# Optimization experiments

Hardware: AMD Instinct MI355X
Metric: run time of the kernel (lower is better)

## Reference

```python
import jax, jax.numpy as jnp
import numpy as np

N_NODES = 50000
N_EDGES = 1200000
NODE_DIM = 64
HIDDEN = 64
OUT_DIM = 1
N_LAYERS = 3


def setup_inputs() -> dict:
    key = jax.random.key(0)
    ks = jax.random.split(key, 16)
    inp = {
        "H": jax.random.normal(ks[0], (N_NODES, NODE_DIM), dtype=jnp.float32),
        "edge_index": jax.random.randint(ks[1], (2, N_EDGES), 0, N_NODES, dtype=jnp.int64),
        "E": jax.random.normal(ks[2], (N_EDGES, 16), dtype=jnp.float32),
    }
    # per-layer params: node_encoder (enc) and update_w (upd); weights stored [in, out]
    for i in range(N_LAYERS):
        in_dim = NODE_DIM if i == 0 else HIDDEN
        s = 1.0 / np.sqrt(in_dim)
        inp[f"enc_w{i}"] = jax.random.uniform(ks[3 + 2 * i], (in_dim, HIDDEN), jnp.float32, -s, s)
        inp[f"enc_b{i}"] = jax.random.uniform(ks[4 + 2 * i], (HIDDEN,), jnp.float32, -s, s)
        sh = 1.0 / np.sqrt(HIDDEN)
        inp[f"upd_w{i}"] = jax.random.uniform(ks[9 + 2 * i], (HIDDEN, HIDDEN), jnp.float32, -sh, sh)
        inp[f"upd_b{i}"] = jax.random.uniform(ks[10 + 2 * i], (HIDDEN,), jnp.float32, -sh, sh)
    so = 1.0 / np.sqrt(HIDDEN)
    inp["out_w"] = jax.random.uniform(ks[15], (HIDDEN, OUT_DIM), jnp.float32, -so, so)
    inp["out_b"] = jnp.zeros((OUT_DIM,), jnp.float32)
    return inp


def _gcn_forward(H, edge_index, params):
    u, v = edge_index[0], edge_index[1]
    # symmetric normalization with implicit self-loop degree bump (calc_norm_factor)
    deg = jax.ops.segment_sum(jnp.ones(u.shape[0], H.dtype), u, num_segments=N_NODES) + 1.0
    dis = deg ** -0.5  # deg >= 1, never inf
    norm = dis[u] * dis[v]  # [n_edges]
    for i in range(N_LAYERS):
        enc_w, enc_b, upd_w, upd_b = params[i]
        H = H @ enc_w + enc_b                      # node_encoder
        msgs = norm[:, None] * H[u]                # gather + scale
        agg = jax.ops.segment_sum(msgs, v, num_segments=N_NODES)  # scatter-add
        H = jax.nn.relu((agg + H) @ upd_w + upd_b)  # update + ReLU (dropout = identity in eval)
    return H


def reference(H, edge_index, E, enc_w0, enc_b0, upd_w0, upd_b0, enc_w1, enc_b1,
              upd_w1, upd_b1, enc_w2, enc_b2, upd_w2, upd_b2, out_w, out_b):
    params = [(enc_w0, enc_b0, upd_w0, upd_b0),
              (enc_w1, enc_b1, upd_w1, upd_b1),
              (enc_w2, enc_b2, upd_w2, upd_b2)]
    Hf = _gcn_forward(H, edge_index, params)
    graph_emb = jnp.mean(Hf, axis=0, keepdims=True)  # [1, HIDDEN] readout (batch=None)
    return graph_emb @ out_w + out_b                 # [1, OUT_DIM]
```

## Files before the change

kernel.cpp:

```cpp
#include <hip/hip_runtime.h>
#include <hip/hip_fp16.h>

#define NN 50000
#define NE 1200000
#define DIM 64
#define NB 782
#define BB 196
#define SLICES 512
#define ES 2344
#define VCAP 2048
#define GB 782
#define FRONT_LDS 33792


__device__ __forceinline__ void lsort_body(char* smem, const int* __restrict__ ei,
                                           ushort* __restrict__ usort,
                                           int* __restrict__ ebuf,
                                           int* __restrict__ lpart_u,
                                           int* __restrict__ lpart_v,
                                           int s) {
    int* hist = (int*)smem;
    int* wsum = (int*)(smem + 3136);
    ushort* sbu = (ushort*)(smem + 4160);
    int* sbv = (int*)(smem + 8848);
    int t = threadIdx.x;
    int w = t >> 6, l = t & 63;
    int e0 = s * ES, e1 = min(e0 + ES, NE), len = e1 - e0;
    int i0 = t * 4;

    for (int i = t; i < NB; i += 256) hist[i] = 0;
    __syncthreads();
    for (int e = e0 + t; e < e1; e += 256) atomicAdd(&hist[ei[e] >> 6], 1);
    __syncthreads();
    {
        int h0 = (i0 + 0 < NB) ? hist[i0 + 0] : 0;
        int h1 = (i0 + 1 < NB) ? hist[i0 + 1] : 0;
        int h2 = (i0 + 2 < NB) ? hist[i0 + 2] : 0;
        int h3 = (i0 + 3 < NB) ? hist[i0 + 3] : 0;
        int p1 = h0, p2 = h0 + h1, p3 = p2 + h2, p4 = p3 + h3;
        int inc = p4;
        for (int o = 1; o < 64; o <<= 1) {
            int x = __shfl_up(inc, o, 64);
            if (l >= o) inc += x;
        }
        if (l == 63) wsum[w] = inc;
        __syncthreads();
        int base = 0;
#pragma unroll
        for (int j = 0; j < 4; ++j) if (j < w) base += wsum[j];
        int total = wsum[0] + wsum[1] + wsum[2] + wsum[3];
        int excl = base + inc - p4;
        int* lpu = lpart_u + s * (NB + 1);
        if (i0 + 0 < NB) { lpu[i0 + 0] = excl;      hist[i0 + 0] = excl; }
        if (i0 + 1 < NB) { lpu[i0 + 1] = excl + p1; hist[i0 + 1] = excl + p1; }
        if (i0 + 2 < NB) { lpu[i0 + 2] = excl + p2; hist[i0 + 2] = excl + p2; }
        if (i0 + 3 < NB) { lpu[i0 + 3] = excl + p3; hist[i0 + 3] = excl + p3; }
        if (t == 255) lpu[NB] = total;
    }
    __syncthreads();
    for (int e = e0 + t; e < e1; e += 256) {
        int u = ei[e];
        int pos = atomicAdd(&hist[u >> 6], 1);
        sbu[pos] = (ushort)u;
    }
    __syncthreads();
    for (int i = t; i < len; i += 256) usort[e0 + i] = sbu[i];
    for (int i = t; i < NB; i += 256) hist[i] = 0;
    __syncthreads();

    for (int e = e0 + t; e < e1; e += 256) atomicAdd(&hist[ei[NE + e] >> 6], 1);
    __syncthreads();
    {
        int h0 = (i0 + 0 < NB) ? hist[i0 + 0] : 0;
        int h1 = (i0 + 1 < NB) ? hist[i0 + 1] : 0;
        int h2 = (i0 + 2 < NB) ? hist[i0 + 2] : 0;
        int h3 = (i0 + 3 < NB) ? hist[i0 + 3] : 0;
        int p1 = h0, p2 = h0 + h1, p3 = p2 + h2, p4 = p3 + h3;
        int inc = p4;
        for (int o = 1; o < 64; o <<= 1) {
            int x = __shfl_up(inc, o, 64);
            if (l >= o) inc += x;
        }
        if (l == 63) wsum[w] = inc;
        __syncthreads();
        int base = 0;
#pragma unroll
        for (int j = 0; j < 4; ++j) if (j < w) base += wsum[j];
        int total = wsum[0] + wsum[1] + wsum[2] + wsum[3];
        int excl = base + inc - p4;
        int* lpv = lpart_v + s * (NB + 1);
        if (i0 + 0 < NB) { lpv[i0 + 0] = excl;      hist[i0 + 0] = excl; }
        if (i0 + 1 < NB) { lpv[i0 + 1] = excl + p1; hist[i0 + 1] = excl + p1; }
        if (i0 + 2 < NB) { lpv[i0 + 2] = excl + p2; hist[i0 + 2] = excl + p2; }
        if (i0 + 3 < NB) { lpv[i0 + 3] = excl + p3; hist[i0 + 3] = excl + p3; }
        if (t == 255) lpv[NB] = total;
    }
    __syncthreads();
    for (int e = e0 + t; e < e1; e += 256) {
        int u = ei[e], v = ei[NE + e];
        int pos = atomicAdd(&hist[v >> 6], 1);
        sbv[pos] = u | ((v & 63) << 16);
    }
    __syncthreads();
    for (int i = t; i < len; i += 256) ebuf[e0 + i] = sbv[i];
}

__device__ __forceinline__ void gemm_h_body(char* smem, int blk,
                                            const float* __restrict__ A,
                                            const float* __restrict__ W,
                                            const float* __restrict__ bias,
                                            __half* __restrict__ Ch, int M) {
    float (*As)[68] = (float(*)[68])smem;
    float (*Bs)[64] = (float(*)[64])(smem + 17408);
    int t = threadIdx.x;
    int row0 = blk * 64;
#pragma unroll
    for (int i = 0; i < 4; ++i) {
        int idx = t + i * 256;
        int r = idx >> 4, c = (idx & 15) << 2;
        float4 val = make_float4(0.f, 0.f, 0.f, 0.f);
        if (row0 + r < M) val = *(const float4*)&A[(size_t)(row0 + r) * DIM + c];
        *(float4*)&As[r][c] = val;
        *(float4*)&Bs[r][c] = *(const float4*)&W[r * DIM + c];
    }
    __syncthreads();
    int r0 = (t >> 4) * 4;
    int c0 = (t & 15) * 4;
    float acc[4][4] = {};
#pragma unroll
    for (int k = 0; k < 64; k += 4) {
        float4 b0 = *(float4*)&Bs[k + 0][c0];
        float4 b1 = *(float4*)&Bs[k + 1][c0];
        float4 b2 = *(float4*)&Bs[k + 2][c0];
        float4 b3 = *(float4*)&Bs[k + 3][c0];
#pragma unroll
        for (int i = 0; i < 4; ++i) {
            float4 av = *(float4*)&As[r0 + i][k];
            acc[i][0] = fmaf(av.x, b0.x, fmaf(av.y, b1.x, fmaf(av.z, b2.x, fmaf(av.w, b3.x, acc[i][0]))));
            acc[i][1] = fmaf(av.x, b0.y, fmaf(av.y, b1.y, fmaf(av.z, b2.y, fmaf(av.w, b3.y, acc[i][1]))));
            acc[i][2] = fmaf(av.x, b0.z, fmaf(av.y, b1.z, fmaf(av.z, b2.z, fmaf(av.w, b3.z, acc[i][2]))));
            acc[i][3] = fmaf(av.x, b0.w, fmaf(av.y, b1.w, fmaf(av.z, b2.w, fmaf(av.w, b3.w, acc[i][3]))));
        }
    }
    float4 bv = *(const float4*)&bias[c0];
#pragma unroll
    for (int i = 0; i < 4; ++i) {
        int r = row0 + r0 + i;
        if (r < M) {
            __half2 p0 = __floats2half2_rn(acc[i][0] + bv.x, acc[i][1] + bv.y);
            __half2 p1 = __floats2half2_rn(acc[i][2] + bv.z, acc[i][3] + bv.w);
            uint2 pk;
            pk.x = *(unsigned int*)&p0;
            pk.y = *(unsigned int*)&p1;
            *(uint2*)&Ch[(size_t)r * DIM + c0] = pk;
        }
    }
}

__global__ __launch_bounds__(256) void k_front(const int* __restrict__ ei,
                                               ushort* __restrict__ usort,
                                               int* __restrict__ ebuf,
                                               int* __restrict__ lpart_u,
                                               int* __restrict__ lpart_v,
                                               const float* __restrict__ A,
                                               const float* __restrict__ W,
                                               const float* __restrict__ bias,
                                               __half* __restrict__ Ch) {
    extern __shared__ char smem[];
    int b = blockIdx.x;
    if (b < 256)
        lsort_body(smem, ei, usort, ebuf, lpart_u, lpart_v, b);
    else if (b < 512)
        gemm_h_body(smem, b - 256, A, W, bias, Ch, NN);
    else if (b < 768)
        lsort_body(smem, ei, usort, ebuf, lpart_u, lpart_v, b - 256);
    else
        gemm_h_body(smem, b - 512, A, W, bias, Ch, NN);
}

__global__ __launch_bounds__(256) void k_mid(const ushort* __restrict__ usort,
                                             const int* __restrict__ lpart_u,
                                             float* __restrict__ dis,
                                             float* __restrict__ colsum) {
    __shared__ int sh[4][64];
    int bid = blockIdx.x;
    if (bid == 0 && threadIdx.x < 64) colsum[threadIdx.x] = 0.f;
    int w = threadIdx.x >> 6, l = threadIdx.x & 63;
    int b = bid * 4 + w;
    if (b >= NB) return;
    sh[w][l] = 0;
    __builtin_amdgcn_wave_barrier();
    for (int s = l; s < SLICES; s += 64) {
        const int* row = lpart_u + s * (NB + 1);
        int st = row[b], en = row[b + 1];
        for (int i = st; i < en; ++i)
            atomicAdd(&sh[w][usort[s * ES + i] & 63], 1);
    }
    __builtin_amdgcn_wave_barrier();
    int n = (b << 6) + l;
    if (n < NN) dis[n] = rsqrtf((float)sh[w][l] + 1.0f);
}

__global__ __launch_bounds__(256) void k_vsort(const int* __restrict__ ebuf,
                                               const int* __restrict__ lpart_v,
                                               const float* __restrict__ dis,
                                               int* __restrict__ edges,
                                               int* __restrict__ row_ptr) {
    __shared__ int cache[4][VCAP];
    __shared__ int cnt[4][64];
    __shared__ int cur[4][64];
    int w = threadIdx.x >> 6, l = threadIdx.x & 63;
    int b = blockIdx.x * 4 + w;
    if (b >= NB) return;
    int len[8], st8[8];
    int tl = 0, ts = 0;
#pragma unroll
    for (int k = 0; k < 8; ++k) {
        const int* row = lpart_v + (l * 8 + k) * (NB + 1);
        int st = row[b], en = row[b + 1];
        st8[k] = st;
        len[k] = en - st;
        tl += len[k];
        ts += st;
    }
    int n = tl, rb = ts;
    for (int off = 32; off; off >>= 1) {
        n += __shfl_down(n, off, 64);
        rb += __shfl_down(rb, off, 64);
    }
    n = __shfl(n, 0, 64);
    int rbase = __shfl(rb, 0, 64);
    cnt[w][l] = 0;
    __builtin_amdgcn_wave_barrier();
    if (n <= VCAP) {
        int inc = tl;
        for (int o = 1; o < 64; o <<= 1) {
            int x = __shfl_up(inc, o, 64);
            if (l >= o) inc += x;
        }
        int pos = inc - tl;
#pragma unroll
        for (int k = 0; k < 8; ++k) {
            int s = l * 8 + k;
            int st = st8[k];
            for (int i = 0; i < len[k]; ++i)
                cache[w][pos++] = ebuf[s * ES + st + i];
        }
        __builtin_amdgcn_wave_barrier();
        for (int i = l; i < n; i += 64)
            atomicAdd(&cnt[w][(cache[w][i] >> 16) & 63], 1);
        __builtin_amdgcn_wave_barrier();
        int c = cnt[w][l];
        int inc2 = c;
        for (int o = 1; o < 64; o <<= 1) {
            int x = __shfl_up(inc2, o, 64);
            if (l >= o) inc2 += x;
        }
        int excl = inc2 - c;
        cur[w][l] = rbase + excl;
        row_ptr[(b << 6) + l] = rbase + excl;
        __builtin_amdgcn_wave_barrier();
        for (int i = l; i < n; i += 64) {
            int rec = cache[w][i];
            int u = rec & 0xFFFF;
            int p2 = atomicAdd(&cur[w][(rec >> 16) & 63], 1);
            ushort dh = __half_as_ushort(__float2half_rn(dis[u]));
            edges[p2] = u | ((int)dh << 16);
        }
    } else {
        for (int s = l; s < SLICES; s += 64) {
            const int* row = lpart_v + s * (NB + 1);
            int st = row[b], en = row[b + 1];
            for (int i = st; i < en; ++i)
                atomicAdd(&cnt[w][(ebuf[s * ES + i] >> 16) & 63], 1);
        }
        __builtin_amdgcn_wave_barrier();
        int c = cnt[w][l];
        int inc2 = c;
        for (int o = 1; o < 64; o <<= 1) {
            int x = __shfl_up(inc2, o, 64);
            if (l >= o) inc2 += x;
        }
        int excl = inc2 - c;
        cur[w][l] = rbase + excl;
        row_ptr[(b << 6) + l] = rbase + excl;
        __builtin_amdgcn_wave_barrier();
        for (int s = l; s < SLICES; s += 64) {
            const int* row = lpart_v + s * (NB + 1);
            int st = row[b], en = row[b + 1];
            for (int i = st; i < en; ++i) {
                int rec = ebuf[s * ES + i];
                int u = rec & 0xFFFF;
                int p2 = atomicAdd(&cur[w][(rec >> 16) & 63], 1);
                ushort dh = __half_as_ushort(__float2half_rn(dis[u]));
                edges[p2] = u | ((int)dh << 16);
            }
        }
    }
}

__global__ __launch_bounds__(256) void k_gemm2(const float* __restrict__ X,
                                               const float* __restrict__ W1,
                                               const float* __restrict__ b1,
                                               const float* __restrict__ W2,
                                               const float* __restrict__ b2,
                                               __half* __restrict__ Zh, int M) {
    __shared__ float As[64][68];
    __shared__ float Bs[64][64];
    int t = threadIdx.x;
    int row0 = blockIdx.x * 64;
#pragma unroll
    for (int i = 0; i < 4; ++i) {
        int idx = t + i * 256;
        int r = idx >> 4, c = (idx & 15) << 2;
        float4 val = make_float4(0.f, 0.f, 0.f, 0.f);
        if (row0 + r < M) val = *(const float4*)&X[(size_t)(row0 + r) * DIM + c];
        *(float4*)&As[r][c] = val;
        *(float4*)&Bs[r][c] = *(const float4*)&W1[r * DIM + c];
    }
    __syncthreads();
    int r0 = (t >> 4) * 4;
    int c0 = (t & 15) * 4;
    float acc[4][4] = {};
#pragma unroll
    for (int k = 0; k < 64; k += 4) {
        float4 v0 = *(float4*)&Bs[k + 0][c0];
        float4 v1 = *(float4*)&Bs[k + 1][c0];
        float4 v2 = *(float4*)&Bs[k + 2][c0];
        float4 v3 = *(float4*)&Bs[k + 3][c0];
#pragma unroll
        for (int i = 0; i < 4; ++i) {
            float4 av = *(float4*)&As[r0 + i][k];
            acc[i][0] = fmaf(av.x, v0.x, fmaf(av.y, v1.x, fmaf(av.z, v2.x, fmaf(av.w, v3.x, acc[i][0]))));
            acc[i][1] = fmaf(av.x, v0.y, fmaf(av.y, v1.y, fmaf(av.z, v2.y, fmaf(av.w, v3.y, acc[i][1]))));
            acc[i][2] = fmaf(av.x, v0.z, fmaf(av.y, v1.z, fmaf(av.z, v2.z, fmaf(av.w, v3.z, acc[i][2]))));
            acc[i][3] = fmaf(av.x, v0.w, fmaf(av.y, v1.w, fmaf(av.z, v2.w, fmaf(av.w, v3.w, acc[i][3]))));
        }
    }
    float4 bv1 = *(const float4*)&b1[c0];
    __syncthreads();
#pragma unroll
    for (int i = 0; i < 4; ++i) {
        float4 y;
        y.x = fmaxf(acc[i][0] + bv1.x, 0.f);
        y.y = fmaxf(acc[i][1] + bv1.y, 0.f);
        y.z = fmaxf(acc[i][2] + bv1.z, 0.f);
        y.w = fmaxf(acc[i][3] + bv1.w, 0.f);
        *(float4*)&As[r0 + i][c0] = y;
    }
#pragma unroll
    for (int i = 0; i < 4; ++i) {
        int idx = t + i * 256;
        int r = idx >> 4, c = (idx & 15) << 2;
        *(float4*)&Bs[r][c] = *(const float4*)&W2[r * DIM + c];
    }
    __syncthreads();
    float acc2[4][4] = {};
#pragma unroll
    for (int k = 0; k < 64; k += 4) {
        float4 v0 = *(float4*)&Bs[k + 0][c0];
        float4 v1 = *(float4*)&Bs[k + 1][c0];
        float4 v2 = *(float4*)&Bs[k + 2][c0];
        float4 v3 = *(float4*)&Bs[k + 3][c0];
#pragma unroll
        for (int i = 0; i < 4; ++i) {
            float4 av = *(float4*)&As[r0 + i][k];
            acc2[i][0] = fmaf(av.x, v0.x, fmaf(av.y, v1.x, fmaf(av.z, v2.x, fmaf(av.w, v3.x, acc2[i][0]))));
            acc2[i][1] = fmaf(av.x, v0.y, fmaf(av.y, v1.y, fmaf(av.z, v2.y, fmaf(av.w, v3.y, acc2[i][1]))));
            acc2[i][2] = fmaf(av.x, v0.z, fmaf(av.y, v1.z, fmaf(av.z, v2.z, fmaf(av.w, v3.z, acc2[i][2]))));
            acc2[i][3] = fmaf(av.x, v0.w, fmaf(av.y, v1.w, fmaf(av.z, v2.w, fmaf(av.w, v3.w, acc2[i][3]))));
        }
    }
    float4 bv2 = *(const float4*)&b2[c0];
#pragma unroll
    for (int i = 0; i < 4; ++i) {
        int r = row0 + r0 + i;
        if (r < M) {
            __half2 p0 = __floats2half2_rn(acc2[i][0] + bv2.x, acc2[i][1] + bv2.y);
            __half2 p1 = __floats2half2_rn(acc2[i][2] + bv2.z, acc2[i][3] + bv2.w);
            uint2 pk;
            pk.x = *(unsigned int*)&p0;
            pk.y = *(unsigned int*)&p1;
            *(uint2*)&Zh[(size_t)r * DIM + c0] = pk;
        }
    }
}

__global__ __launch_bounds__(256) void k_gemm_last(const float* __restrict__ A,
                                                   const float* __restrict__ W,
                                                   const float* __restrict__ bias,
                                                   int M, float* __restrict__ colsum) {
    __shared__ float As[64][68];
    __shared__ float Bs[64][64];
    int t = threadIdx.x;
    int row0 = blockIdx.x * 64;
#pragma unroll
    for (int i = 0; i < 4; ++i) {
        int idx = t + i * 256;
        int r = idx >> 4, c = (idx & 15) << 2;
        float4 val = make_float4(0.f, 0.f, 0.f, 0.f);
        if (row0 + r < M) val = *(const float4*)&A[(size_t)(row0 + r) * DIM + c];
        *(float4*)&As[r][c] = val;
        *(float4*)&Bs[r][c] = *(const float4*)&W[r * DIM + c];
    }
    __syncthreads();
    int r0 = (t >> 4) * 4;
    int c0 = (t & 15) * 4;
    float acc[4][4] = {};
#pragma unroll
    for (int k = 0; k < 64; k += 4) {
        float4 b0 = *(float4*)&Bs[k + 0][c0];
        float4 b1 = *(float4*)&Bs[k + 1][c0];
        float4 b2 = *(float4*)&Bs[k + 2][c0];
        float4 b3 = *(float4*)&Bs[k + 3][c0];
#pragma unroll
        for (int i = 0; i < 4; ++i) {
            float4 av = *(float4*)&As[r0 + i][k];
            acc[i][0] = fmaf(av.x, b0.x, fmaf(av.y, b1.x, fmaf(av.z, b2.x, fmaf(av.w, b3.x, acc[i][0]))));
            acc[i][1] = fmaf(av.x, b0.y, fmaf(av.y, b1.y, fmaf(av.z, b2.y, fmaf(av.w, b3.y, acc[i][1]))));
            acc[i][2] = fmaf(av.x, b0.z, fmaf(av.y, b1.z, fmaf(av.z, b2.z, fmaf(av.w, b3.z, acc[i][2]))));
            acc[i][3] = fmaf(av.x, b0.w, fmaf(av.y, b1.w, fmaf(av.z, b2.w, fmaf(av.w, b3.w, acc[i][3]))));
        }
    }
    float4 bv = *(const float4*)&bias[c0];
    float csum[4] = {0.f, 0.f, 0.f, 0.f};
#pragma unroll
    for (int i = 0; i < 4; ++i) {
        int r = row0 + r0 + i;
        if (r < M) {
            csum[0] += fmaxf(acc[i][0] + bv.x, 0.f);
            csum[1] += fmaxf(acc[i][1] + bv.y, 0.f);
            csum[2] += fmaxf(acc[i][2] + bv.z, 0.f);
            csum[3] += fmaxf(acc[i][3] + bv.w, 0.f);
        }
    }
    float* red = &As[0][0];
    __syncthreads();
    *(float4*)&red[(t >> 4) * 64 + c0] = make_float4(csum[0], csum[1], csum[2], csum[3]);
    __syncthreads();
    if (t < 64) {
        float s = 0.f;
#pragma unroll
        for (int g = 0; g < 16; ++g) s += red[g * 64 + t];
        atomicAdd(&colsum[t], s);
    }
}

__global__ __launch_bounds__(256) void k_agg(const uint4* __restrict__ Hq4,
                                             const float* __restrict__ dis,
                                             const int* __restrict__ row_ptr,
                                             const int* __restrict__ edges,
                                             float* __restrict__ X) {
    __shared__ int se[4][64];
    int w = threadIdx.x >> 6, l = threadIdx.x & 63;
    int node = (blockIdx.x << 2) + w;
    if (node >= NN) return;
    int start = row_ptr[node];
    int num = row_ptr[node + 1] - start;
    int g = l >> 3;
    int p = l & 7;
    float4 a0 = {0.f, 0.f, 0.f, 0.f};
    float4 a1 = {0.f, 0.f, 0.f, 0.f};
    for (int base = 0; base < num; base += 64) {
        int lim = min(64, num - base);
        se[w][l] = (l < lim) ? edges[start + base + l] : 0;
        __builtin_amdgcn_wave_barrier();
        int octs = (lim + 7) >> 3;
        int rr[8]; uint4 hh[8];
#pragma unroll
        for (int q = 0; q < 8; ++q)
            if (q < octs) rr[q] = se[w][8 * q + g];
#pragma unroll
        for (int q = 0; q < 8; ++q)
            if (q < octs) hh[q] = Hq4[((rr[q] & 0xFFFF) << 3) + p];
#pragma unroll
        for (int q = 0; q < 8; ++q)
            if (q < octs) {
                float wt = __half2float(__ushort_as_half((ushort)((unsigned)rr[q] >> 16)));
                float2 f0 = __half22float2(*(const __half2*)&hh[q].x);
                float2 f1 = __half22float2(*(const __half2*)&hh[q].y);
                float2 f2 = __half22float2(*(const __half2*)&hh[q].z);
                float2 f3 = __half22float2(*(const __half2*)&hh[q].w);
                a0.x = fmaf(wt, f0.x, a0.x);
                a0.y = fmaf(wt, f0.y, a0.y);
                a0.z = fmaf(wt, f1.x, a0.z);
                a0.w = fmaf(wt, f1.y, a0.w);
                a1.x = fmaf(wt, f2.x, a1.x);
                a1.y = fmaf(wt, f2.y, a1.y);
                a1.z = fmaf(wt, f3.x, a1.z);
                a1.w = fmaf(wt, f3.y, a1.w);
            }
        __builtin_amdgcn_wave_barrier();
    }
#pragma unroll
    for (int m = 8; m < 64; m <<= 1) {
        a0.x += __shfl_xor(a0.x, m, 64);
        a0.y += __shfl_xor(a0.y, m, 64);
        a0.z += __shfl_xor(a0.z, m, 64);
        a0.w += __shfl_xor(a0.w, m, 64);
        a1.x += __shfl_xor(a1.x, m, 64);
        a1.y += __shfl_xor(a1.y, m, 64);
        a1.z += __shfl_xor(a1.z, m, 64);
        a1.w += __shfl_xor(a1.w, m, 64);
    }
    if (g == 0) {
        uint4 sv = Hq4[(node << 3) + p];
        float2 s0 = __half22float2(*(const __half2*)&sv.x);
        float2 s1 = __half22float2(*(const __half2*)&sv.y);
        float2 s2 = __half22float2(*(const __half2*)&sv.z);
        float2 s3 = __half22float2(*(const __half2*)&sv.w);
        float dv = dis[node];
        float4 o0, o1;
        o0.x = fmaf(dv, a0.x, s0.x);
        o0.y = fmaf(dv, a0.y, s0.y);
        o0.z = fmaf(dv, a0.z, s1.x);
        o0.w = fmaf(dv, a0.w, s1.y);
        o1.x = fmaf(dv, a1.x, s2.x);
        o1.y = fmaf(dv, a1.y, s2.y);
        o1.z = fmaf(dv, a1.z, s3.x);
        o1.w = fmaf(dv, a1.w, s3.y);
        float* xr = &X[((size_t)node << 6) + (p << 3)];
        *(float4*)xr = o0;
        *(float4*)(xr + 4) = o1;
    }
}

__global__ void k_out(const float* __restrict__ colsum, const float* __restrict__ out_w,
                      const float* __restrict__ out_b, float* __restrict__ out) {
    int f = threadIdx.x;
    float v = colsum[f] * (1.0f / (float)NN) * out_w[f];
    for (int off = 32; off; off >>= 1) v += __shfl_down(v, off, 64);
    if (f == 0) out[0] = v + out_b[0];
}

extern "C" void kernel_launch(void* const* d_in, const int* in_sizes, int n_in,
                              void* d_out, int out_size, void* d_ws, size_t ws_size,
                              hipStream_t stream) {
    const float* H  = (const float*)d_in[0];
    const int*   ei = (const int*)d_in[1];
    const float* enc_w[3] = { (const float*)d_in[3], (const float*)d_in[7],  (const float*)d_in[11] };
    const float* enc_b[3] = { (const float*)d_in[4], (const float*)d_in[8],  (const float*)d_in[12] };
    const float* upd_w[3] = { (const float*)d_in[5], (const float*)d_in[9],  (const float*)d_in[13] };
    const float* upd_b[3] = { (const float*)d_in[6], (const float*)d_in[10], (const float*)d_in[14] };
    const float* out_w = (const float*)d_in[15];
    const float* out_b = (const float*)d_in[16];
    float* out = (float*)d_out;

    size_t off = 0;
    auto carve = [&](size_t bytes) {
        void* p = (char*)d_ws + off;
        off = (off + bytes + 255) & ~(size_t)255;
        return p;
    };
    int*    lpart_u = (int*)carve((size_t)SLICES * (NB + 1) * 4);
    int*    lpart_v = (int*)carve((size_t)SLICES * (NB + 1) * 4);
    float*  dis     = (float*)carve((size_t)NN * 4);
    ushort* usort   = (ushort*)carve((size_t)SLICES * ES * 2);
    int*    ebuf    = (int*)carve((size_t)SLICES * ES * 4);
    int*    edges   = (int*)carve((size_t)NE * 4);
    int*    row_ptr = (int*)carve((size_t)(NN + 65) * 4);
    __half* Ch      = (__half*)carve((size_t)NN * DIM * 2);
    float*  X       = (float*)carve((size_t)NN * DIM * 4);
    float*  colsum  = (float*)carve(64 * 4);

    const int AB = (NN + 3) / 4;
    const uint4* Hq4 = (const uint4*)Ch;

    k_front<<<512 + GB, 256, FRONT_LDS, stream>>>(ei, usort, ebuf, lpart_u, lpart_v,
                                                  H, enc_w[0], enc_b[0], Ch);
    k_mid<<<BB, 256, 0, stream>>>(usort, lpart_u, dis, colsum);
    k_vsort<<<BB, 256, 0, stream>>>(ebuf, lpart_v, dis, edges, row_ptr);

    k_agg<<<AB, 256, 0, stream>>>(Hq4, dis, row_ptr, edges, X);
    k_gemm2<<<GB, 256, 0, stream>>>(X, upd_w[0], upd_b[0], enc_w[1], enc_b[1], Ch, NN);
    k_agg<<<AB, 256, 0, stream>>>(Hq4, dis, row_ptr, edges, X);
    k_gemm2<<<GB, 256, 0, stream>>>(X, upd_w[1], upd_b[1], enc_w[2], enc_b[2], Ch, NN);
    k_agg<<<AB, 256, 0, stream>>>(Hq4, dis, row_ptr, edges, X);
    k_gemm_last<<<GB, 256, 0, stream>>>(X, upd_w[2], upd_b[2], NN, colsum);

    k_out<<<1, 64, 0, stream>>>(colsum, out_w, out_b, out);
}
```

Baseline: 383.5 us.

## Fuse aggregation into following GEMM and widen mid/vsort to block-per-bucket

Merges the per-node sparse aggregation into the subsequent GEMM kernels, so each 64-row block aggregates its nodes straight into shared memory and the fp32 X buffer no longer goes through global memory. Because a block now reads other nodes' features while writing new ones, the half-precision feature buffer is double-buffered (ChA/ChB). k_mid and k_vsort are also restructured from one bucket per wave to one bucket per 256-thread block, which puts more parallelism on the sorting stage. The cost is that each fused block handles 64 nodes serially per wave (16 each), with fewer blocks and a larger LDS footprint, which may lower latency hiding in the gather.

```diff
diff --git a/kernel.cpp b/kernel.cpp
--- a/kernel.cpp
+++ b/kernel.cpp
@@ -5,7 +5,6 @@
 #define NE 1200000
 #define DIM 64
 #define NB 782
-#define BB 196
 #define SLICES 512
 #define ES 2344
 #define VCAP 2048
@@ -182,23 +181,21 @@
                                              const int* __restrict__ lpart_u,
                                              float* __restrict__ dis,
                                              float* __restrict__ colsum) {
-    __shared__ int sh[4][64];
-    int bid = blockIdx.x;
-    if (bid == 0 && threadIdx.x < 64) colsum[threadIdx.x] = 0.f;
-    int w = threadIdx.x >> 6, l = threadIdx.x & 63;
-    int b = bid * 4 + w;
-    if (b >= NB) return;
-    sh[w][l] = 0;
-    __builtin_amdgcn_wave_barrier();
-    for (int s = l; s < SLICES; s += 64) {
+    __shared__ int sh[64];
+    int b = blockIdx.x;
+    int t = threadIdx.x;
+    if (b == 0 && t < 64) colsum[t] = 0.f;
+    if (t < 64) sh[t] = 0;
+    __syncthreads();
+    for (int s = t; s < SLICES; s += 256) {
         const int* row = lpart_u + s * (NB + 1);
         int st = row[b], en = row[b + 1];
         for (int i = st; i < en; ++i)
-            atomicAdd(&sh[w][usort[s * ES + i] & 63], 1);
-    }
-    __builtin_amdgcn_wave_barrier();
-    int n = (b << 6) + l;
-    if (n < NN) dis[n] = rsqrtf((float)sh[w][l] + 1.0f);
+            atomicAdd(&sh[usort[s * ES + i] & 63], 1);
+    }
+    __syncthreads();
+    int n = (b << 6) + t;
+    if (t < 64 && n < NN) dis[n] = rsqrtf((float)sh[t] + 1.0f);
 }
 
 __global__ __launch_bounds__(256) void k_vsort(const int* __restrict__ ebuf,
@@ -206,92 +203,92 @@
                                                const float* __restrict__ dis,
                                                int* __restrict__ edges,
                                                int* __restrict__ row_ptr) {
-    __shared__ int cache[4][VCAP];
-    __shared__ int cnt[4][64];
-    __shared__ int cur[4][64];
-    int w = threadIdx.x >> 6, l = threadIdx.x & 63;
-    int b = blockIdx.x * 4 + w;
-    if (b >= NB) return;
-    int len[8], st8[8];
-    int tl = 0, ts = 0;
-#pragma unroll
-    for (int k = 0; k < 8; ++k) {
-        const int* row = lpart_v + (l * 8 + k) * (NB + 1);
-        int st = row[b], en = row[b + 1];
-        st8[k] = st;
-        len[k] = en - st;
-        tl += len[k];
-        ts += st;
-    }
-    int n = tl, rb = ts;
-    for (int off = 32; off; off >>= 1) {
-        n += __shfl_down(n, off, 64);
-        rb += __shfl_down(rb, off, 64);
-    }
-    n = __shfl(n, 0, 64);
-    int rbase = __shfl(rb, 0, 64);
-    cnt[w][l] = 0;
-    __builtin_amdgcn_wave_barrier();
+    __shared__ int cache[VCAP];
+    __shared__ int cnt[64];
+    __shared__ int cur[64];
+    __shared__ int wsum[4];
+    __shared__ int rsum[4];
+    int t = threadIdx.x, w = t >> 6, l = t & 63;
+    int b = blockIdx.x;
+    int s0 = t * 2, s1 = t * 2 + 1;
+    const int* r0p = lpart_v + s0 * (NB + 1);
+    const int* r1p = lpart_v + s1 * (NB + 1);
+    int a0 = r0p[b], a1 = r0p[b + 1];
+    int c0 = r1p[b], c1 = r1p[b + 1];
+    int len0 = a1 - a0, len1 = c1 - c0;
+    int tl = len0 + len1;
+    int ts = a0 + c0;
+    int inc = tl;
+    for (int o = 1; o < 64; o <<= 1) {
+        int x = __shfl_up(inc, o, 64);
+        if (l >= o) inc += x;
+    }
+    int tss = ts;
+    for (int off = 32; off; off >>= 1) tss += __shfl_down(tss, off, 64);
+    if (l == 63) wsum[w] = inc;
+    if (l == 0) rsum[w] = tss;
+    if (t < 64) cnt[t] = 0;
+    __syncthreads();
+    int base = 0;
+#pragma unroll
+    for (int j = 0; j < 4; ++j) if (j < w) base += wsum[j];
+    int n = wsum[0] + wsum[1] + wsum[2] + wsum[3];
+    int rbase = rsum[0] + rsum[1] + rsum[2] + rsum[3];
+    int pos = base + inc - tl;
     if (n <= VCAP) {
-        int inc = tl;
-        for (int o = 1; o < 64; o <<= 1) {
-            int x = __shfl_up(inc, o, 64);
-            if (l >= o) inc += x;
-        }
-        int pos = inc - tl;
-#pragma unroll
-        for (int k = 0; k < 8; ++k) {
-            int s = l * 8 + k;
-            int st = st8[k];
-            for (int i = 0; i < len[k]; ++i)
-                cache[w][pos++] = ebuf[s * ES + st + i];
-        }
-        __builtin_amdgcn_wave_barrier();
-        for (int i = l; i < n; i += 64)
-            atomicAdd(&cnt[w][(cache[w][i] >> 16) & 63], 1);
-        __builtin_amdgcn_wave_barrier();
-        int c = cnt[w][l];
-        int inc2 = c;
-        for (int o = 1; o < 64; o <<= 1) {
-            int x = __shfl_up(inc2, o, 64);
-            if (l >= o) inc2 += x;
-        }
-        int excl = inc2 - c;
-        cur[w][l] = rbase + excl;
-        row_ptr[(b << 6) + l] = rbase + excl;
-        __builtin_amdgcn_wave_barrier();
-        for (int i = l; i < n; i += 64) {
-            int rec = cache[w][i];
+        for (int i = 0; i < len0; ++i) cache[pos + i] = ebuf[s0 * ES + a0 + i];
+        int pos1 = pos + len0;
+        for (int i = 0; i < len1; ++i) cache[pos1 + i] = ebuf[s1 * ES + c0 + i];
+        __syncthreads();
+        for (int i = t; i < n; i += 256)
+            atomicAdd(&cnt[(cache[i] >> 16) & 63], 1);
+        __syncthreads();
+        if (w == 0) {
+            int c = cnt[l];
+            int inc2 = c;
+            for (int o = 1; o < 64; o <<= 1) {
+                int x = __shfl_up(inc2, o, 64);
+                if (l >= o) inc2 += x;
+            }
+            int excl = inc2 - c;
+            cur[l] = rbase + excl;
+            row_ptr[(b << 6) + l] = rbase + excl;
+        }
+        __syncthreads();
+        for (int i = t; i < n; i += 256) {
+            int rec = cache[i];
             int u = rec & 0xFFFF;
-            int p2 = atomicAdd(&cur[w][(rec >> 16) & 63], 1);
+            int p2 = atomicAdd(&cur[(rec >> 16) & 63], 1);
             ushort dh = __half_as_ushort(__float2half_rn(dis[u]));
             edges[p2] = u | ((int)dh << 16);
         }
     } else {
-        for (int s = l; s < SLICES; s += 64) {
+        for (int s = t; s < SLICES; s += 256) {
             const int* row = lpart_v + s * (NB + 1);
             int st = row[b], en = row[b + 1];
             for (int i = st; i < en; ++i)
-                atomicAdd(&cnt[w][(ebuf[s * ES + i] >> 16) & 63], 1);
-        }
-        __builtin_amdgcn_wave_barrier();
-        int c = cnt[w][l];
-        int inc2 = c;
-        for (int o = 1; o < 64; o <<= 1) {
-            int x = __shfl_up(inc2, o, 64);
-            if (l >= o) inc2 += x;
-        }
-        int excl = inc2 - c;
-        cur[w][l] = rbase + excl;
-        row_ptr[(b << 6) + l] = rbase + excl;
-        __builtin_amdgcn_wave_barrier();
-        for (int s = l; s < SLICES; s += 64) {
+                atomicAdd(&cnt[(ebuf[s * ES + i] >> 16) & 63], 1);
+        }
+        __syncthreads();
+        if (w == 0) {
+            int c = cnt[l];
+            int inc2 = c;
+            for (int o = 1; o < 64; o <<= 1) {
+                int x = __shfl_up(inc2, o, 64);
+                if (l >= o) inc2 += x;
+            }
+            int excl = inc2 - c;
+            cur[l] = rbase + excl;
+            row_ptr[(b << 6) + l] = rbase + excl;
+        }
+        __syncthreads();
+        for (int s = t; s < SLICES; s += 256) {
             const int* row = lpart_v + s * (NB + 1);
             int st = row[b], en = row[b + 1];
             for (int i = st; i < en; ++i) {
                 int rec = ebuf[s * ES + i];
                 int u = rec & 0xFFFF;
-                int p2 = atomicAdd(&cur[w][(rec >> 16) & 63], 1);
+                int p2 = atomicAdd(&cur[(rec >> 16) & 63], 1);
                 ushort dh = __half_as_ushort(__float2half_rn(dis[u]));
                 edges[p2] = u | ((int)dh << 16);
             }
@@ -299,23 +296,113 @@
     }
 }
 
-__global__ __launch_bounds__(256) void k_gemm2(const float* __restrict__ X,
-                                               const float* __restrict__ W1,
-                                               const float* __restrict__ b1,
-                                               const float* __restrict__ W2,
-                                               const float* __restrict__ b2,
-                                               __half* __restrict__ Zh, int M) {
+__device__ __forceinline__ void agg_body(float (*As)[68], int (*se)[64],
+                                         const uint4* __restrict__ Hq4,
+                                         const float* __restrict__ dis,
+                                         const int* __restrict__ row_ptr,
+                                         const int* __restrict__ edges,
+                                         int row0) {
+    int t = threadIdx.x;
+    int w = t >> 6, l = t & 63;
+    int g = l >> 3;
+    int p = l & 7;
+#pragma unroll 1
+    for (int nn = 0; nn < 16; ++nn) {
+        int node = row0 + (w << 4) + nn;
+        int start = 0, num = 0;
+        if (node < NN) { start = row_ptr[node]; num = row_ptr[node + 1] - start; }
+        float4 a0 = {0.f, 0.f, 0.f, 0.f};
+        float4 a1 = {0.f, 0.f, 0.f, 0.f};
+        for (int base = 0; base < num; base += 64) {
+            int lim = min(64, num - base);
+            se[w][l] = (l < lim) ? edges[start + base + l] : 0;
+            __builtin_amdgcn_wave_barrier();
+            int octs = (lim + 7) >> 3;
+            int rr[8]; uint4 hh[8];
+#pragma unroll
+            for (int q = 0; q < 8; ++q)
+                if (q < octs) rr[q] = se[w][8 * q + g];
+#pragma unroll
+            for (int q = 0; q < 8; ++q)
+                if (q < octs) hh[q] = Hq4[((rr[q] & 0xFFFF) << 3) + p];
+#pragma unroll
+            for (int q = 0; q < 8; ++q)
+                if (q < octs) {
+                    float wt = __half2float(__ushort_as_half((ushort)((unsigned)rr[q] >> 16)));
+                    float2 f0 = __half22float2(*(const __half2*)&hh[q].x);
+                    float2 f1 = __half22float2(*(const __half2*)&hh[q].y);
+                    float2 f2 = __half22float2(*(const __half2*)&hh[q].z);
+                    float2 f3 = __half22float2(*(const __half2*)&hh[q].w);
+                    a0.x = fmaf(wt, f0.x, a0.x);
+                    a0.y = fmaf(wt, f0.y, a0.y);
+                    a0.z = fmaf(wt, f1.x, a0.z);
+                    a0.w = fmaf(wt, f1.y, a0.w);
+                    a1.x = fmaf(wt, f2.x, a1.x);
+                    a1.y = fmaf(wt, f2.y, a1.y);
+                    a1.z = fmaf(wt, f3.x, a1.z);
+                    a1.w = fmaf(wt, f3.y, a1.w);
+                }
+            __builtin_amdgcn_wave_barrier();
+        }
+#pragma unroll
+        for (int m = 8; m < 64; m <<= 1) {
+            a0.x += __shfl_xor(a0.x, m, 64);
+            a0.y += __shfl_xor(a0.y, m, 64);
+            a0.z += __shfl_xor(a0.z, m, 64);
+            a0.w += __shfl_xor(a0.w, m, 64);
+            a1.x += __shfl_xor(a1.x, m, 64);
+            a1.y += __shfl_xor(a1.y, m, 64);
+            a1.z += __shfl_xor(a1.z, m, 64);
+            a1.w += __shfl_xor(a1.w, m, 64);
+        }
+        if (g == 0) {
+            int r = (w << 4) + nn;
+            if (node < NN) {
+                uint4 sv = Hq4[(node << 3) + p];
+                float2 s0 = __half22float2(*(const __half2*)&sv.x);
+                float2 s1 = __half22float2(*(const __half2*)&sv.y);
+                float2 s2 = __half22float2(*(const __half2*)&sv.z);
+                float2 s3 = __half22float2(*(const __half2*)&sv.w);
+                float dv = dis[node];
+                float4 o0, o1;
+                o0.x = fmaf(dv, a0.x, s0.x);
+                o0.y = fmaf(dv, a0.y, s0.y);
+                o0.z = fmaf(dv, a0.z, s1.x);
+                o0.w = fmaf(dv, a0.w, s1.y);
+                o1.x = fmaf(dv, a1.x, s2.x);
+                o1.y = fmaf(dv, a1.y, s2.y);
+                o1.z = fmaf(dv, a1.z, s3.x);
+                o1.w = fmaf(dv, a1.w, s3.y);
+                *(float4*)&As[r][p << 3] = o0;
+                *(float4*)&As[r][(p << 3) + 4] = o1;
+            } else {
+                float4 z = {0.f, 0.f, 0.f, 0.f};
+                *(float4*)&As[r][p << 3] = z;
+                *(float4*)&As[r][(p << 3) + 4] = z;
+            }
+        }
+    }
+}
+
+__global__ __launch_bounds__(256) void k_aggemm2(const uint4* __restrict__ Hq4,
+                                                 const float* __restrict__ dis,
+                                                 const int* __restrict__ row_ptr,
+                                                 const int* __restrict__ edges,
+                                                 const float* __restrict__ W1,
+                                                 const float* __restrict__ b1,
+                                                 const float* __restrict__ W2,
+                                                 const float* __restrict__ b2,
+                                                 __half* __restrict__ Zh) {
     __shared__ float As[64][68];
     __shared__ float Bs[64][64];
+    __shared__ int se[4][64];
     int t = threadIdx.x;
     int row0 = blockIdx.x * 64;
+    agg_body(As, se, Hq4, dis, row_ptr, edges, row0);
 #pragma unroll
     for (int i = 0; i < 4; ++i) {
         int idx = t + i * 256;
         int r = idx >> 4, c = (idx & 15) << 2;
-        float4 val = make_float4(0.f, 0.f, 0.f, 0.f);
-        if (row0 + r < M) val = *(const float4*)&X[(size_t)(row0 + r) * DIM + c];
-        *(float4*)&As[r][c] = val;
         *(float4*)&Bs[r][c] = *(const float4*)&W1[r * DIM + c];
     }
     __syncthreads();
@@ -375,7 +462,7 @@
 #pragma unroll
     for (int i = 0; i < 4; ++i) {
         int r = row0 + r0 + i;
-        if (r < M) {
+        if (r < NN) {
             __half2 p0 = __floats2half2_rn(acc2[i][0] + bv2.x, acc2[i][1] + bv2.y);
             __half2 p1 = __floats2half2_rn(acc2[i][2] + bv2.z, acc2[i][3] + bv2.w);
             uint2 pk;
@@ -386,21 +473,23 @@
     }
 }
 
-__global__ __launch_bounds__(256) void k_gemm_last(const float* __restrict__ A,
-                                                   const float* __restrict__ W,
-                                                   const float* __restrict__ bias,
-                                                   int M, float* __restrict__ colsum) {
+__global__ __launch_bounds__(256) void k_aggemm_last(const uint4* __restrict__ Hq4,
+                                                     const float* __restrict__ dis,
+                                                     const int* __restrict__ row_ptr,
+                                                     const int* __restrict__ edges,
+                                                     const float* __restrict__ W,
+                                                     const float* __restrict__ bias,
+                                                     float* __restrict__ colsum) {
     __shared__ float As[64][68];
     __shared__ float Bs[64][64];
+    __shared__ int se[4][64];
     int t = threadIdx.x;
     int row0 = blockIdx.x * 64;
+    agg_body(As, se, Hq4, dis, row_ptr, edges, row0);
 #pragma unroll
     for (int i = 0; i < 4; ++i) {
         int idx = t + i * 256;
         int r = idx >> 4, c = (idx & 15) << 2;
-        float4 val = make_float4(0.f, 0.f, 0.f, 0.f);
-        if (row0 + r < M) val = *(const float4*)&A[(size_t)(row0 + r) * DIM + c];
-        *(float4*)&As[r][c] = val;
         *(float4*)&Bs[r][c] = *(const float4*)&W[r * DIM + c];
     }
     __syncthreads();
@@ -427,7 +516,7 @@
 #pragma unroll
     for (int i = 0; i < 4; ++i) {
         int r = row0 + r0 + i;
-        if (r < M) {
+        if (r < NN) {
             csum[0] += fmaxf(acc[i][0] + bv.x, 0.f);
             csum[1] += fmaxf(acc[i][1] + bv.y, 0.f);
             csum[2] += fmaxf(acc[i][2] + bv.z, 0.f);
@@ -443,85 +532,6 @@
 #pragma unroll
         for (int g = 0; g < 16; ++g) s += red[g * 64 + t];
         atomicAdd(&colsum[t], s);
-    }
-}
-
-__global__ __launch_bounds__(256) void k_agg(const uint4* __restrict__ Hq4,
-                                             const float* __restrict__ dis,
-                                             const int* __restrict__ row_ptr,
-                                             const int* __restrict__ edges,
-                                             float* __restrict__ X) {
-    __shared__ int se[4][64];
-    int w = threadIdx.x >> 6, l = threadIdx.x & 63;
-    int node = (blockIdx.x << 2) + w;
-    if (node >= NN) return;
-    int start = row_ptr[node];
-    int num = row_ptr[node + 1] - start;
-    int g = l >> 3;
-    int p = l & 7;
-    float4 a0 = {0.f, 0.f, 0.f, 0.f};
-    float4 a1 = {0.f, 0.f, 0.f, 0.f};
-    for (int base = 0; base < num; base += 64) {
-        int lim = min(64, num - base);
-        se[w][l] = (l < lim) ? edges[start + base + l] : 0;
-        __builtin_amdgcn_wave_barrier();
-        int octs = (lim + 7) >> 3;
-        int rr[8]; uint4 hh[8];
-#pragma unroll
-        for (int q = 0; q < 8; ++q)
-            if (q < octs) rr[q] = se[w][8 * q + g];
-#pragma unroll
-        for (int q = 0; q < 8; ++q)
-            if (q < octs) hh[q] = Hq4[((rr[q] & 0xFFFF) << 3) + p];
-#pragma unroll
-        for (int q = 0; q < 8; ++q)
-            if (q < octs) {
-                float wt = __half2float(__ushort_as_half((ushort)((unsigned)rr[q] >> 16)));
-                float2 f0 = __half22float2(*(const __half2*)&hh[q].x);
-                float2 f1 = __half22float2(*(const __half2*)&hh[q].y);
-                float2 f2 = __half22float2(*(const __half2*)&hh[q].z);
-                float2 f3 = __half22float2(*(const __half2*)&hh[q].w);
-                a0.x = fmaf(wt, f0.x, a0.x);
-                a0.y = fmaf(wt, f0.y, a0.y);
-                a0.z = fmaf(wt, f1.x, a0.z);
-                a0.w = fmaf(wt, f1.y, a0.w);
-                a1.x = fmaf(wt, f2.x, a1.x);
-                a1.y = fmaf(wt, f2.y, a1.y);
-                a1.z = fmaf(wt, f3.x, a1.z);
-                a1.w = fmaf(wt, f3.y, a1.w);
-            }
-        __builtin_amdgcn_wave_barrier();
-    }
-#pragma unroll
-    for (int m = 8; m < 64; m <<= 1) {
-        a0.x += __shfl_xor(a0.x, m, 64);
-        a0.y += __shfl_xor(a0.y, m, 64);
-        a0.z += __shfl_xor(a0.z, m, 64);
-        a0.w += __shfl_xor(a0.w, m, 64);
-        a1.x += __shfl_xor(a1.x, m, 64);
-        a1.y += __shfl_xor(a1.y, m, 64);
-        a1.z += __shfl_xor(a1.z, m, 64);
-        a1.w += __shfl_xor(a1.w, m, 64);
-    }
-    if (g == 0) {
-        uint4 sv = Hq4[(node << 3) + p];
-        float2 s0 = __half22float2(*(const __half2*)&sv.x);
-        float2 s1 = __half22float2(*(const __half2*)&sv.y);
-        float2 s2 = __half22float2(*(const __half2*)&sv.z);
-        float2 s3 = __half22float2(*(const __half2*)&sv.w);
-        float dv = dis[node];
-        float4 o0, o1;
-        o0.x = fmaf(dv, a0.x, s0.x);
-        o0.y = fmaf(dv, a0.y, s0.y);
-        o0.z = fmaf(dv, a0.z, s1.x);
-        o0.w = fmaf(dv, a0.w, s1.y);
-        o1.x = fmaf(dv, a1.x, s2.x);
-        o1.y = fmaf(dv, a1.y, s2.y);
-        o1.z = fmaf(dv, a1.z, s3.x);
-        o1.w = fmaf(dv, a1.w, s3.y);
-        float* xr = &X[((size_t)node << 6) + (p << 3)];
-        *(float4*)xr = o0;
-        *(float4*)(xr + 4) = o1;
     }
 }
 
@@ -559,24 +569,24 @@
     int*    ebuf    = (int*)carve((size_t)SLICES * ES * 4);
     int*    edges   = (int*)carve((size_t)NE * 4);
     int*    row_ptr = (int*)carve((size_t)(NN + 65) * 4);
-    __half* Ch      = (__half*)carve((size_t)NN * DIM * 2);
-    float*  X       = (float*)carve((size_t)NN * DIM * 4);
+    __half* ChA     = (__half*)carve((size_t)NN * DIM * 2);
+    __half* ChB     = (__half*)carve((size_t)NN * DIM * 2);
     float*  colsum  = (float*)carve(64 * 4);
 
-    const int AB = (NN + 3) / 4;
-    const uint4* Hq4 = (const uint4*)Ch;
+    const uint4* HqA = (const uint4*)ChA;
+    const uint4* HqB = (const uint4*)ChB;
 
     k_front<<<512 + GB, 256, FRONT_LDS, stream>>>(ei, usort, ebuf, lpart_u, lpart_v,
-                                                  H, enc_w[0], enc_b[0], Ch);
-    k_mid<<<BB, 256, 0, stream>>>(usort, lpart_u, dis, colsum);
-    k_vsort<<<BB, 256, 0, stream>>>(ebuf, lpart_v, dis, edges, row_ptr);
-
-    k_agg<<<AB, 256, 0, stream>>>(Hq4, dis, row_ptr, edges, X);
-    k_gemm2<<<GB, 256, 0, stream>>>(X, upd_w[0], upd_b[0], enc_w[1], enc_b[1], Ch, NN);
-    k_agg<<<AB, 256, 0, stream>>>(Hq4, dis, row_ptr, edges, X);
-    k_gemm2<<<GB, 256, 0, stream>>>(X, upd_w[1], upd_b[1], enc_w[2], enc_b[2], Ch, NN);
-    k_agg<<<AB, 256, 0, stream>>>(Hq4, dis, row_ptr, edges, X);
-    k_gemm_last<<<GB, 256, 0, stream>>>(X, upd_w[2], upd_b[2], NN, colsum);
+                                                  H, enc_w[0], enc_b[0], ChA);
+    k_mid<<<NB, 256, 0, stream>>>(usort, lpart_u, dis, colsum);
+    k_vsort<<<NB, 256, 0, stream>>>(ebuf, lpart_v, dis, edges, row_ptr);
+
+    k_aggemm2<<<GB, 256, 0, stream>>>(HqA, dis, row_ptr, edges,
+                                      upd_w[0], upd_b[0], enc_w[1], enc_b[1], ChB);
+    k_aggemm2<<<GB, 256, 0, stream>>>(HqB, dis, row_ptr, edges,
+                                      upd_w[1], upd_b[1], enc_w[2], enc_b[2], ChA);
+    k_aggemm_last<<<GB, 256, 0, stream>>>(HqA, dis, row_ptr, edges,
+                                          upd_w[2], upd_b[2], colsum);
 
     k_out<<<1, 64, 0, stream>>>(colsum, out_w, out_b, out);
 }
```

After: 599.0 us. 1.56x slower.
